# Kernel optimization log

Measured on AMD Instinct MI355X. Metric: run time of the kernel, lower is better.

Reference implementation:

```python
import jax, jax.numpy as jnp
import numpy as np
from jax import lax

B, L, H, E = 2, 96, 2, 63
OUT = 256            # out_channels of q/k linear projections
CONV1, CONV2, KS = 64, 128, 3
C = E + 1 + CONV2    # 192 augmented channels (original + time + conv)
LT = L - KS + 1      # 94  truncated length after kernel-3 'valid' conv
LL = 2 * LT          # 188 lead-lag (length-doubled) path
N = LL - 1           # 187 streamed-signature length
SIG = C + C * C      # 37056 depth-2 signature channels
EV = 64              # value feature dim
DN = ('NCH', 'OIH', 'NCH')


def setup_inputs() -> dict:
    key = jax.random.key(0)
    ks = jax.random.split(key, 16)
    w = lambda k, shape, fan: jax.random.normal(k, shape, jnp.float32) / np.sqrt(fan)
    return {
        'q': jax.random.normal(ks[0], (B, L, H, E), jnp.float32),
        'k': jax.random.normal(ks[1], (B, L, H, E), jnp.float32),
        'v': jax.random.normal(ks[2], (B, H, N, EV), jnp.float32),
        'Wq1': w(ks[3], (CONV1, E, KS), E * KS), 'bq1': jnp.zeros((CONV1,), jnp.float32),
        'Wq2': w(ks[4], (CONV2, CONV1, 1), CONV1), 'bq2': jnp.zeros((CONV2,), jnp.float32),
        'Wk1': w(ks[5], (CONV1, E, KS), E * KS), 'bk1': jnp.zeros((CONV1,), jnp.float32),
        'Wk2': w(ks[6], (CONV2, CONV1, 1), CONV1), 'bk2': jnp.zeros((CONV2,), jnp.float32),
        'Wlq': w(ks[7], (OUT, SIG), SIG), 'blq': jnp.zeros((OUT,), jnp.float32),
        'Wlk': w(ks[8], (OUT, SIG), SIG), 'blk': jnp.zeros((OUT,), jnp.float32),
        'mask': jnp.zeros((1, 1), jnp.bool_),
    }


def _augment(x, W1, b1, W2, b2):
    # x: [BH, L, E] -> [BH, LT, C]; pieces: truncated original, time, conv stack.
    trunc = x[:, KS - 1:, :]                                  # [BH, LT, E]
    t = jnp.linspace(0.0, 1.0, LT, dtype=jnp.float32)
    time = jnp.broadcast_to(t[None, :, None], (x.shape[0], LT, 1))
    xc = x.transpose(0, 2, 1)                                 # [BH, E, L]
    y = lax.conv_general_dilated(xc, W1, (1,), 'VALID', dimension_numbers=DN) + b1[None, :, None]
    y = jax.nn.relu(lax.conv_general_dilated(y, W2, (1,), 'VALID', dimension_numbers=DN) + b2[None, :, None])
    return jnp.concatenate([trunc, time, y.transpose(0, 2, 1)], axis=2)  # [BH, LT, C]


def _lead_lag(x):
    # [BH, M, C] -> interleave lead/lag -> [BH, 2M, C]
    lag = jnp.concatenate([x[:, 1:], x[:, -1:]], axis=1)
    return jnp.stack([x, lag], axis=2).reshape(x.shape[0], 2 * x.shape[1], x.shape[2])


def _sig_stream2(path):
    # Streamed depth-2 path signature of path [BH, LL, C] -> [BH, N, C + C^2].
    dx = jnp.diff(path, axis=1)                               # [BH, N, C]
    s1 = jnp.cumsum(dx, axis=1)                               # level-1 stream
    pre = s1 - dx                                             # exclusive prefix X_j - X_0
    # per-step level-2 increment: (P_j + dx_j/2) (x) dx_j
    term = (pre + 0.5 * dx)[:, :, :, None] * dx[:, :, None, :]  # [BH, N, C, C]
    s2 = jnp.cumsum(term, axis=1).reshape(dx.shape[0], dx.shape[1], C * C)
    return jnp.concatenate([s1, s2], axis=-1)                 # [BH, N, SIG]


def reference(q, k, v, Wq1, bq1, Wq2, bq2, Wk1, bk1, Wk2, bk2, Wlq, blq, Wlk, blk, mask):
    BH = B * H
    qh = q.transpose(0, 2, 1, 3).reshape(BH, L, E)
    kh = k.transpose(0, 2, 1, 3).reshape(BH, L, E)
    q_sig = _sig_stream2(_lead_lag(_augment(qh, Wq1, bq1, Wq2, bq2)))  # [BH, N, SIG]
    k_sig = _sig_stream2(_lead_lag(_augment(kh, Wk1, bk1, Wk2, bk2)))
    q_proj = jnp.einsum('bns,os->bno', q_sig, Wlq) + blq              # [BH, N, OUT]
    k_proj = jnp.einsum('bns,os->bno', k_sig, Wlk) + blk
    attn = jnp.tanh(jnp.einsum('bxe,bye->bxy', q_proj, k_proj))       # [BH, N, N]
    attn = attn.reshape(B, H, N, N)
    out = jnp.einsum('bhxy,bhye->bhxe', attn, v)                      # [B, H, N, EV]
    return out
```

## Files before the change

### kernel.cpp

```cpp
#include <hip/hip_runtime.h>
#include <hip/hip_bf16.h>

constexpr int kB   = 2;
constexpr int kL   = 96;
constexpr int kH   = 2;
constexpr int kE   = 63;
constexpr int kOUT = 256;
constexpr int kC1  = 64;
constexpr int kC2  = 128;
constexpr int kKS  = 3;
constexpr int kC   = 192;
constexpr int kLT  = 94;
constexpr int kN   = 187;
constexpr int kTAU = 93;
constexpr int kEV  = 64;
constexpr int kBH  = 4;
constexpr int kSIG = 37056;
constexpr int kNCOL = kBH * kTAU;

constexpr int NSTEP = 193;
constexpr int ISPL  = 16;
constexpr int NTILES = 6;

constexpr size_t AUG_OFF  = 0;
constexpr size_t AUG_SZ   = (size_t)2 * kBH * kLT * kC;
constexpr size_t D_OFF    = AUG_OFF + AUG_SZ;
constexpr size_t D_SZ     = (size_t)2 * kBH * kTAU * kC;
constexpr size_t U_OFF    = D_OFF + D_SZ;
constexpr size_t F_OFF    = U_OFF + D_SZ;
constexpr size_t F_SZ     = (size_t)2 * kBH * kTAU * kOUT;

typedef __attribute__((ext_vector_type(8))) short short8;
typedef __attribute__((ext_vector_type(4))) float f32x4;

typedef const float __attribute__((address_space(1)))* gptr_t;
typedef float __attribute__((address_space(3)))* lptr_t;

__device__ __forceinline__ unsigned int fbits(float f) { return __float_as_uint(f); }
__device__ __forceinline__ float bitsf(unsigned int u) { return __uint_as_float(u); }

__device__ __forceinline__ unsigned short f2bf(float x) {
    unsigned int u = __float_as_uint(x);
    unsigned int r = (u + 0x7FFFu + ((u >> 16) & 1u)) >> 16;
    return (unsigned short)r;
}
__device__ __forceinline__ float bfbits2f(unsigned short u) {
    return bitsf(((unsigned int)u) << 16);
}

union Pack8 { unsigned int u[4]; short8 v; };

__device__ __forceinline__ void split_rne8(float4 x0, float4 x1, short8& hi, short8& lo) {
    float xf[8] = {x0.x, x0.y, x0.z, x0.w, x1.x, x1.y, x1.z, x1.w};
    Pack8 ph, pl;
    #pragma unroll
    for (int p = 0; p < 4; p++) {
        unsigned short ha = f2bf(xf[2 * p]), hb = f2bf(xf[2 * p + 1]);
        ph.u[p] = (unsigned int)ha | ((unsigned int)hb << 16);
        unsigned short la = f2bf(xf[2 * p] - bfbits2f(ha));
        unsigned short lb = f2bf(xf[2 * p + 1] - bfbits2f(hb));
        pl.u[p] = (unsigned int)la | ((unsigned int)lb << 16);
    }
    hi = ph.v; lo = pl.v;
}

__global__ __launch_bounds__(192) void augment_kernel(
    const float* __restrict__ q, const float* __restrict__ k,
    const float* __restrict__ W1q, const float* __restrict__ b1q,
    const float* __restrict__ W2q, const float* __restrict__ b2q,
    const float* __restrict__ W1k, const float* __restrict__ b1k,
    const float* __restrict__ W2k, const float* __restrict__ b2k,
    float* __restrict__ aug)
{
    const int t  = blockIdx.x;
    const int bh = blockIdx.y;
    const int qk = blockIdx.z;
    const int tid = threadIdx.x;

    const float* x  = qk ? k   : q;
    const float* W1 = qk ? W1k : W1q;
    const float* b1 = qk ? b1k : b1q;
    const float* W2 = qk ? W2k : W2q;
    const float* b2 = qk ? b2k : b2q;

    __shared__ float xwin[kKS][kE];
    __shared__ float hbuf[kC1];

    const int b = bh >> 1, h = bh & 1;
    if (tid < kKS * kE) {
        int s = tid / kE, e = tid - s * kE;
        xwin[s][e] = x[(((size_t)b * kL + (t + s)) * kH + h) * kE + e];
    }
    __syncthreads();

    if (tid < kC1) {
        float acc = b1[tid];
        const float* wrow = W1 + (size_t)tid * kE * kKS;
        #pragma unroll 3
        for (int s = 0; s < kKS; s++)
            for (int e = 0; e < kE; e++)
                acc += xwin[s][e] * wrow[e * kKS + s];
        hbuf[tid] = acc;
    }
    __syncthreads();

    float* augrow = aug + ((size_t)(qk * kBH + bh) * kLT + t) * kC;
    if (tid < kC2) {
        float acc = b2[tid];
        const float* wrow = W2 + (size_t)tid * kC1;
        for (int o1 = 0; o1 < kC1; o1++)
            acc += hbuf[o1] * wrow[o1];
        augrow[kE + 1 + tid] = fmaxf(acc, 0.0f);
    }
    if (tid < kE) augrow[tid] = xwin[kKS - 1][tid];
    if (tid == kE) augrow[kE] = (float)t * (1.0f / 93.0f);
}

__global__ __launch_bounds__(192) void diffcum_kernel(
    const float* __restrict__ aug, float* __restrict__ dArr, float* __restrict__ uArr)
{
    const int bh = blockIdx.x, qk = blockIdx.y;
    const int c = threadIdx.x;
    const float* a = aug + (size_t)(qk * kBH + bh) * kLT * kC;
    float* dp = dArr + (size_t)(qk * kBH + bh) * kTAU * kC;
    float* up = uArr + (size_t)(qk * kBH + bh) * kTAU * kC;
    float run = 0.f;
    float prev = a[c];
    #pragma unroll 4
    for (int tau = 0; tau < kTAU; tau++) {
        float nxt = a[(size_t)(tau + 1) * kC + c];
        float dd = nxt - prev;
        run += dd;
        dp[(size_t)tau * kC + c] = dd;
        up[(size_t)tau * kC + c] = run - 0.5f * dd;
        prev = nxt;
    }
}

__global__ __launch_bounds__(256) void sigproj_kernel(
    const float* __restrict__ Wlq,
    const float* __restrict__ Wlk,
    const float* __restrict__ dArr,
    const float* __restrict__ uArr,
    float* __restrict__ F)
{
    const int otile = blockIdx.x;
    const int ntile = blockIdx.y;
    const int zz = blockIdx.z;
    const int qk = zz / ISPL;
    const int is = zz - qk * ISPL;

    const float* __restrict__ W = qk ? Wlk : Wlq;
    const float* dB = dArr + (size_t)qk * kNCOL * kC;
    const float* uB = uArr + (size_t)qk * kNCOL * kC;

    __shared__ __align__(16) float Ws[64][196];

    const int tid  = threadIdx.x;
    const int lane = tid & 63;
    const int w    = tid >> 6;
    const int quad = lane >> 4;
    const int l16  = lane & 15;
    const int orow = (w & 1) * 32;
    const int ncol = (w >> 1) * 32;

    const int sbase = NSTEP / ISPL, srem = NSTEP % ISPL;
    const int s0 = is * sbase + (is < srem ? is : srem);
    const int ns = sbase + (is < srem ? 1 : 0);

    short8 bh_r[2][6], bl_r[2][6];
    const float* uptr[2];
    float nmask[2];
    #pragma unroll
    for (int b = 0; b < 2; b++) {
        const int n = ntile * 64 + ncol + b * 16 + l16;
        const bool nv = n < kNCOL;
        nmask[b] = nv ? 1.f : 0.f;
        const float* dn = dB + (size_t)(nv ? n : 0) * kC;
        uptr[b] = uB + (size_t)(nv ? n : 0) * kC;
        #pragma unroll
        for (int jb = 0; jb < 6; jb++) {
            float4 x0 = *reinterpret_cast<const float4*>(dn + jb * 32 + quad * 8);
            float4 x1 = *reinterpret_cast<const float4*>(dn + jb * 32 + quad * 8 + 4);
            if (!nv) { x0 = make_float4(0, 0, 0, 0); x1 = make_float4(0, 0, 0, 0); }
            split_rne8(x0, x1, bh_r[b][jb], bl_r[b][jb]);
        }
    }

    f32x4 acc[2][2];
    #pragma unroll
    for (int a = 0; a < 2; a++)
        #pragma unroll
        for (int b = 0; b < 2; b++)
            acc[a][b] = (f32x4){0.f, 0.f, 0.f, 0.f};

    const int row0 = w * 16;
    const float* gbase = W + (size_t)(otile * 64 + row0) * kSIG + lane * 4;

    for (int ci = 0; ci < ns; ci++) {
        const int s = s0 + ci;
        const int col0 = 192 * s;

        __syncthreads();
        if (lane < 48) {
            const float* gp = gbase + col0;
            #pragma unroll
            for (int i = 0; i < 16; i++)
                __builtin_amdgcn_global_load_lds(
                    (gptr_t)(gp + (size_t)i * kSIG),
                    (lptr_t)&Ws[row0 + i][0], 16, 0, 0);
        }
        __syncthreads();

        float uscale[2];
        #pragma unroll
        for (int b = 0; b < 2; b++)
            uscale[b] = (s == 0) ? nmask[b] : uptr[b][s - 1] * nmask[b];

        f32x4 tmp[2][2];
        #pragma unroll
        for (int a = 0; a < 2; a++)
            #pragma unroll
            for (int b = 0; b < 2; b++)
                tmp[a][b] = (f32x4){0.f, 0.f, 0.f, 0.f};

        #pragma unroll
        for (int jb = 0; jb < 6; jb++) {
            short8 ah[2], al[2];
            #pragma unroll
            for (int a = 0; a < 2; a++) {
                const float* lr = &Ws[orow + a * 16 + l16][jb * 32 + quad * 8];
                float4 w0 = *reinterpret_cast<const float4*>(lr);
                float4 w1 = *reinterpret_cast<const float4*>(lr + 4);
                split_rne8(w0, w1, ah[a], al[a]);
            }
            #pragma unroll
            for (int a = 0; a < 2; a++)
                #pragma unroll
                for (int b = 0; b < 2; b++) {
                    tmp[a][b] = __builtin_amdgcn_mfma_f32_16x16x32_bf16(
                        ah[a], bh_r[b][jb], tmp[a][b], 0, 0, 0);
                    tmp[a][b] = __builtin_amdgcn_mfma_f32_16x16x32_bf16(
                        ah[a], bl_r[b][jb], tmp[a][b], 0, 0, 0);
                    tmp[a][b] = __builtin_amdgcn_mfma_f32_16x16x32_bf16(
                        al[a], bh_r[b][jb], tmp[a][b], 0, 0, 0);
                }
        }

        #pragma unroll
        for (int a = 0; a < 2; a++)
            #pragma unroll
            for (int b = 0; b < 2; b++)
                #pragma unroll
                for (int r = 0; r < 4; r++)
                    acc[a][b][r] += uscale[b] * tmp[a][b][r];
    }

    #pragma unroll
    for (int a = 0; a < 2; a++) {
        const int o = otile * 64 + orow + a * 16 + quad * 4;
        #pragma unroll
        for (int b = 0; b < 2; b++) {
            const int n = ntile * 64 + ncol + b * 16 + l16;
            if (n < kNCOL) {
                float* dst = F + ((size_t)qk * kNCOL + n) * kOUT + o;
                #pragma unroll
                for (int r = 0; r < 4; r++)
                    atomicAdd(dst + r, acc[a][b][r]);
            }
        }
    }
}

__global__ __launch_bounds__(256) void cumsum_kernel(
    float* __restrict__ F,
    const float* __restrict__ blq, const float* __restrict__ blk)
{
    const int bh = blockIdx.x, qk = blockIdx.y;
    const int o = threadIdx.x;
    float run = (qk ? blk : blq)[o];
    float* base = F + ((size_t)qk * kNCOL + bh * kTAU) * kOUT + o;
    #pragma unroll 8
    for (int tau = 0; tau < kTAU; tau++) {
        run += base[(size_t)tau * kOUT];
        base[(size_t)tau * kOUT] = run;
    }
}

__device__ __forceinline__ float tanh_fast(float x) {
    return 1.f - 2.f / (__expf(2.f * x) + 1.f);
}

__global__ __launch_bounds__(128) void attn_kernel(
    const float* __restrict__ P, const float* __restrict__ v,
    float* __restrict__ out)
{
    const int sg = blockIdx.x;
    const int bh = blockIdx.y;
    const int tid = threadIdx.x;

    __shared__ float q_l[kOUT];
    __shared__ __align__(16) float kp_l[kTAU][65];
    __shared__ float A_l[kTAU];

    const float* qrow = P + ((size_t)bh * kTAU + sg) * kOUT;
    q_l[tid] = qrow[tid];
    q_l[tid + 128] = qrow[tid + 128];

    const float* kbase = P + ((size_t)kNCOL + bh * kTAU) * kOUT;
    const int ri = tid >> 6;
    const int oi = tid & 63;
    float dot = 0.f;
    for (int oc = 0; oc < kOUT; oc += 64) {
        __syncthreads();
        for (int t = ri; t < kTAU; t += 2)
            kp_l[t][oi] = kbase[(size_t)t * kOUT + oc + oi];
        __syncthreads();
        if (tid < kTAU) {
            #pragma unroll 8
            for (int i = 0; i < 64; i++)
                dot += q_l[oc + i] * kp_l[tid][i];
        }
    }
    if (tid < kTAU) A_l[tid] = tanh_fast(dot);
    __syncthreads();

    if (tid < kEV) {
        const float* vb = v + (size_t)bh * kN * kEV + tid;
        float acc2 = 0.f;
        #pragma unroll 4
        for (int t = 0; t < kTAU - 1; t++)
            acc2 += A_l[t] * (vb[(size_t)(2 * t) * kEV] + vb[(size_t)(2 * t + 1) * kEV]);
        acc2 += A_l[kTAU - 1] * (vb[(size_t)184 * kEV] + vb[(size_t)185 * kEV] +
                                 vb[(size_t)186 * kEV]);
        const size_t rb = (size_t)bh * kN;
        out[(rb + 2 * sg) * kEV + tid] = acc2;
        out[(rb + 2 * sg + 1) * kEV + tid] = acc2;
        if (sg == kTAU - 1) out[(rb + 186) * kEV + tid] = acc2;
    }
}

extern "C" void kernel_launch(void* const* d_in, const int* in_sizes, int n_in,
                              void* d_out, int out_size, void* d_ws, size_t ws_size,
                              hipStream_t stream)
{
    (void)in_sizes; (void)n_in; (void)out_size; (void)ws_size;
    auto fp = [&](int i) { return (const float*)d_in[i]; };

    float* ws   = (float*)d_ws;
    float* aug  = ws + AUG_OFF;
    float* dArr = ws + D_OFF;
    float* uArr = ws + U_OFF;
    float* F    = ws + F_OFF;

    hipMemsetAsync(F, 0, F_SZ * sizeof(float), stream);

    augment_kernel<<<dim3(kLT, kBH, 2), 192, 0, stream>>>(
        fp(0), fp(1), fp(3), fp(4), fp(5), fp(6), fp(7), fp(8), fp(9), fp(10), aug);
    diffcum_kernel<<<dim3(kBH, 2), 192, 0, stream>>>(aug, dArr, uArr);
    sigproj_kernel<<<dim3(4, NTILES, 2 * ISPL), 256, 0, stream>>>(
        fp(11), fp(13), dArr, uArr, F);
    cumsum_kernel<<<dim3(kBH, 2), 256, 0, stream>>>(F, fp(12), fp(14));
    attn_kernel<<<dim3(kTAU, kBH), 128, 0, stream>>>(F, fp(2), (float*)d_out);
}
```

Measured before the change: 300.6 us.

## Cover all columns per block so each weight tile is read once

Restructures the signature-projection GEMM so each block handles a 32-row output tile against all 372 columns with 8 waves, removing the column-tile grid dimension. Weight slices are fetched from global memory once per output tile instead of once per column tile. The fp32 to bf16 hi/lo split of each weight slice is done once into shared memory and shared by all waves. In exchange there are fewer, larger blocks, an extra barrier per step, and a serialized stage-convert-compute pattern per step.

```diff
diff --git a/kernel.cpp b/kernel.cpp
--- a/kernel.cpp
+++ b/kernel.cpp
@@ -18,9 +18,7 @@
 constexpr int kSIG = 37056;
 constexpr int kNCOL = kBH * kTAU;
 
-constexpr int NSTEP = 193;
-constexpr int ISPL  = 16;
-constexpr int NTILES = 6;
+constexpr int SPL = 16;
 
 constexpr size_t AUG_OFF  = 0;
 constexpr size_t AUG_SZ   = (size_t)2 * kBH * kLT * kC;
@@ -137,7 +135,7 @@
     }
 }
 
-__global__ __launch_bounds__(256) void sigproj_kernel(
+__global__ __launch_bounds__(512) void sigproj_kernel(
     const float* __restrict__ Wlq,
     const float* __restrict__ Wlk,
     const float* __restrict__ dArr,
@@ -145,128 +143,143 @@
     float* __restrict__ F)
 {
     const int otile = blockIdx.x;
-    const int ntile = blockIdx.y;
-    const int zz = blockIdx.z;
-    const int qk = zz / ISPL;
-    const int is = zz - qk * ISPL;
+    const int zz = blockIdx.y;
+    const int qk = zz / SPL;
+    const int is = zz - qk * SPL;
 
     const float* __restrict__ W = qk ? Wlk : Wlq;
     const float* dB = dArr + (size_t)qk * kNCOL * kC;
     const float* uB = uArr + (size_t)qk * kNCOL * kC;
 
-    __shared__ __align__(16) float Ws[64][196];
+    __shared__ __align__(16) float stage[32 * 196];
+    __shared__ __align__(16) unsigned short WhiS[32 * 200];
+    __shared__ __align__(16) unsigned short WloS[32 * 200];
 
     const int tid  = threadIdx.x;
+    const int w    = tid >> 6;
     const int lane = tid & 63;
-    const int w    = tid >> 6;
     const int quad = lane >> 4;
     const int l16  = lane & 15;
-    const int orow = (w & 1) * 32;
-    const int ncol = (w >> 1) * 32;
-
-    const int sbase = NSTEP / ISPL, srem = NSTEP % ISPL;
-    const int s0 = is * sbase + (is < srem ? is : srem);
-    const int ns = sbase + (is < srem ? 1 : 0);
-
-    short8 bh_r[2][6], bl_r[2][6];
-    const float* uptr[2];
-    float nmask[2];
+
+    const int s0 = (is == 0) ? 0 : 12 * is + 1;
+    const int ns = (is == 0) ? 13 : 12;
+
+    short8 bh_r[3][6], bl_r[3][6];
+    const float* uptr[3];
+    float nmask[3];
     #pragma unroll
-    for (int b = 0; b < 2; b++) {
-        const int n = ntile * 64 + ncol + b * 16 + l16;
+    for (int f = 0; f < 3; f++) {
+        const int n = w * 48 + f * 16 + l16;
         const bool nv = n < kNCOL;
-        nmask[b] = nv ? 1.f : 0.f;
+        nmask[f] = nv ? 1.f : 0.f;
         const float* dn = dB + (size_t)(nv ? n : 0) * kC;
-        uptr[b] = uB + (size_t)(nv ? n : 0) * kC;
+        uptr[f] = uB + (size_t)(nv ? n : 0) * kC;
         #pragma unroll
         for (int jb = 0; jb < 6; jb++) {
             float4 x0 = *reinterpret_cast<const float4*>(dn + jb * 32 + quad * 8);
             float4 x1 = *reinterpret_cast<const float4*>(dn + jb * 32 + quad * 8 + 4);
             if (!nv) { x0 = make_float4(0, 0, 0, 0); x1 = make_float4(0, 0, 0, 0); }
-            split_rne8(x0, x1, bh_r[b][jb], bl_r[b][jb]);
-        }
-    }
-
-    f32x4 acc[2][2];
+            split_rne8(x0, x1, bh_r[f][jb], bl_r[f][jb]);
+        }
+    }
+
+    f32x4 acc[2][3];
     #pragma unroll
     for (int a = 0; a < 2; a++)
         #pragma unroll
-        for (int b = 0; b < 2; b++)
-            acc[a][b] = (f32x4){0.f, 0.f, 0.f, 0.f};
-
-    const int row0 = w * 16;
-    const float* gbase = W + (size_t)(otile * 64 + row0) * kSIG + lane * 4;
+        for (int f = 0; f < 3; f++)
+            acc[a][f] = (f32x4){0.f, 0.f, 0.f, 0.f};
+
+    const int row0 = w * 4;
+    const float* gbase = W + (size_t)(otile * 32 + row0) * kSIG + lane * 4;
 
     for (int ci = 0; ci < ns; ci++) {
         const int s = s0 + ci;
-        const int col0 = 192 * s;
-
-        __syncthreads();
+
+        __syncthreads();
+
         if (lane < 48) {
-            const float* gp = gbase + col0;
-            #pragma unroll
-            for (int i = 0; i < 16; i++)
+            const float* gp = gbase + (size_t)192 * s;
+            #pragma unroll
+            for (int i = 0; i < 4; i++)
                 __builtin_amdgcn_global_load_lds(
                     (gptr_t)(gp + (size_t)i * kSIG),
-                    (lptr_t)&Ws[row0 + i][0], 16, 0, 0);
-        }
-        __syncthreads();
-
-        float uscale[2];
-        #pragma unroll
-        for (int b = 0; b < 2; b++)
-            uscale[b] = (s == 0) ? nmask[b] : uptr[b][s - 1] * nmask[b];
-
-        f32x4 tmp[2][2];
+                    (lptr_t)&stage[(row0 + i) * 196], 16, 0, 0);
+        }
+        __syncthreads();
+
+        if (tid < 384) {
+            const int r = tid & 31, cb = tid >> 5;
+            const float* src = &stage[r * 196 + cb * 16];
+            float4 x0 = *reinterpret_cast<const float4*>(src);
+            float4 x1 = *reinterpret_cast<const float4*>(src + 4);
+            float4 x2 = *reinterpret_cast<const float4*>(src + 8);
+            float4 x3 = *reinterpret_cast<const float4*>(src + 12);
+            short8 h0, l0, h1, l1;
+            split_rne8(x0, x1, h0, l0);
+            split_rne8(x2, x3, h1, l1);
+            const int o16 = r * 200 + cb * 16;
+            *reinterpret_cast<short8*>(&WhiS[o16]) = h0;
+            *reinterpret_cast<short8*>(&WhiS[o16 + 8]) = h1;
+            *reinterpret_cast<short8*>(&WloS[o16]) = l0;
+            *reinterpret_cast<short8*>(&WloS[o16 + 8]) = l1;
+        }
+        __syncthreads();
+
+        float uscale[3];
+        #pragma unroll
+        for (int f = 0; f < 3; f++)
+            uscale[f] = (s == 0) ? nmask[f] : uptr[f][s - 1] * nmask[f];
+
+        f32x4 tmp[2][3];
         #pragma unroll
         for (int a = 0; a < 2; a++)
             #pragma unroll
-            for (int b = 0; b < 2; b++)
-                tmp[a][b] = (f32x4){0.f, 0.f, 0.f, 0.f};
+            for (int f = 0; f < 3; f++)
+                tmp[a][f] = (f32x4){0.f, 0.f, 0.f, 0.f};
 
         #pragma unroll
         for (int jb = 0; jb < 6; jb++) {
             short8 ah[2], al[2];
             #pragma unroll
             for (int a = 0; a < 2; a++) {
-                const float* lr = &Ws[orow + a * 16 + l16][jb * 32 + quad * 8];
-                float4 w0 = *reinterpret_cast<const float4*>(lr);
-                float4 w1 = *reinterpret_cast<const float4*>(lr + 4);
-                split_rne8(w0, w1, ah[a], al[a]);
+                const int off = (a * 16 + l16) * 200 + jb * 32 + quad * 8;
+                ah[a] = *reinterpret_cast<const short8*>(&WhiS[off]);
+                al[a] = *reinterpret_cast<const short8*>(&WloS[off]);
             }
             #pragma unroll
             for (int a = 0; a < 2; a++)
                 #pragma unroll
-                for (int b = 0; b < 2; b++) {
-                    tmp[a][b] = __builtin_amdgcn_mfma_f32_16x16x32_bf16(
-                        ah[a], bh_r[b][jb], tmp[a][b], 0, 0, 0);
-                    tmp[a][b] = __builtin_amdgcn_mfma_f32_16x16x32_bf16(
-                        ah[a], bl_r[b][jb], tmp[a][b], 0, 0, 0);
-                    tmp[a][b] = __builtin_amdgcn_mfma_f32_16x16x32_bf16(
-                        al[a], bh_r[b][jb], tmp[a][b], 0, 0, 0);
+                for (int f = 0; f < 3; f++) {
+                    tmp[a][f] = __builtin_amdgcn_mfma_f32_16x16x32_bf16(
+                        ah[a], bh_r[f][jb], tmp[a][f], 0, 0, 0);
+                    tmp[a][f] = __builtin_amdgcn_mfma_f32_16x16x32_bf16(
+                        ah[a], bl_r[f][jb], tmp[a][f], 0, 0, 0);
+                    tmp[a][f] = __builtin_amdgcn_mfma_f32_16x16x32_bf16(
+                        al[a], bh_r[f][jb], tmp[a][f], 0, 0, 0);
                 }
         }
 
         #pragma unroll
         for (int a = 0; a < 2; a++)
             #pragma unroll
-            for (int b = 0; b < 2; b++)
+            for (int f = 0; f < 3; f++)
                 #pragma unroll
                 for (int r = 0; r < 4; r++)
-                    acc[a][b][r] += uscale[b] * tmp[a][b][r];
+                    acc[a][f][r] += uscale[f] * tmp[a][f][r];
     }
 
     #pragma unroll
     for (int a = 0; a < 2; a++) {
-        const int o = otile * 64 + orow + a * 16 + quad * 4;
-        #pragma unroll
-        for (int b = 0; b < 2; b++) {
-            const int n = ntile * 64 + ncol + b * 16 + l16;
+        const int o = otile * 32 + a * 16 + quad * 4;
+        #pragma unroll
+        for (int f = 0; f < 3; f++) {
+            const int n = w * 48 + f * 16 + l16;
             if (n < kNCOL) {
                 float* dst = F + ((size_t)qk * kNCOL + n) * kOUT + o;
                 #pragma unroll
                 for (int r = 0; r < 4; r++)
-                    atomicAdd(dst + r, acc[a][b][r]);
+                    atomicAdd(dst + r, acc[a][f][r]);
             }
         }
     }
@@ -358,7 +371,7 @@
     augment_kernel<<<dim3(kLT, kBH, 2), 192, 0, stream>>>(
         fp(0), fp(1), fp(3), fp(4), fp(5), fp(6), fp(7), fp(8), fp(9), fp(10), aug);
     diffcum_kernel<<<dim3(kBH, 2), 192, 0, stream>>>(aug, dArr, uArr);
-    sigproj_kernel<<<dim3(4, NTILES, 2 * ISPL), 256, 0, stream>>>(
+    sigproj_kernel<<<dim3(8, 2 * SPL), 512, 0, stream>>>(
         fp(11), fp(13), dArr, uArr, F);
     cumsum_kernel<<<dim3(kBH, 2), 256, 0, stream>>>(F, fp(12), fp(14));
     attn_kernel<<<dim3(kTAU, kBH), 128, 0, stream>>>(F, fp(2), (float*)d_out);
```

New measurement: 267.9 us. 1.12x faster.
